# Kernel tuning notes

Hardware: AMD Instinct MI355X
Metric: run time of the kernel (lower is better)

The kernel has to match this reference:

```python
import jax, jax.numpy as jnp
import numpy as np

N_HEAD = 32
N_KV = 8
D = 2048
HD = D // N_HEAD
FF = 8192
EPS = 1e-5
THETA = 10000.0


def rms_norm(x, g):
    return g * x / jnp.sqrt(jnp.mean(x * x, axis=-1, keepdims=True) + EPS)


def rope(x):
    # x: [B, H, T, hd]; lucidrains interleaved RoPE
    T = x.shape[2]
    inv_freq = 1.0 / (THETA ** (jnp.arange(0, HD, 2, dtype=jnp.float32) / HD))  # [hd/2]
    freqs = jnp.arange(T, dtype=jnp.float32)[:, None] * inv_freq[None, :]       # [T, hd/2]
    freqs = jnp.repeat(freqs, 2, axis=-1)                                        # [T, hd]
    cos, sin = jnp.cos(freqs), jnp.sin(freqs)
    x1 = x[..., ::2]
    x2 = x[..., 1::2]
    rot = jnp.stack([-x2, x1], axis=-1).reshape(x.shape)
    return x * cos + rot * sin


def attention(x, wq, wk, wv, wo):
    B, T, C = x.shape
    q = (x @ wq).reshape(B, T, N_HEAD, HD).transpose(0, 2, 1, 3)  # [B,H,T,hd]
    k = (x @ wk).reshape(B, T, N_KV, HD).transpose(0, 2, 1, 3)    # [B,Hkv,T,hd]
    v = (x @ wv).reshape(B, T, N_KV, HD).transpose(0, 2, 1, 3)
    q = rope(q)
    k = rope(k)
    rep = N_HEAD // N_KV
    k = jnp.repeat(k, rep, axis=1)
    v = jnp.repeat(v, rep, axis=1)
    att = jnp.einsum('bhqd,bhkd->bhqk', q, k) * (1.0 / np.sqrt(HD))
    causal = jnp.tril(jnp.ones((T, T), dtype=bool))
    att = jnp.where(causal[None, None], att, -jnp.inf)
    att = jax.nn.softmax(att, axis=-1)
    y = jnp.einsum('bhqk,bhkd->bhqd', att, v)
    y = y.transpose(0, 2, 1, 3).reshape(B, T, C)
    return y @ wo


def mlp(x, wg, wu, wd):
    return (jax.nn.silu(x @ wg) * (x @ wu)) @ wd


def setup_inputs() -> dict:
    key = jax.random.key(0)
    ks = jax.random.split(key, 9)
    s = lambda fan_in: 1.0 / np.sqrt(fan_in)
    return {
        'x': jax.random.normal(ks[0], (1, 2048, D), dtype=jnp.float32),
        'g1': jnp.ones((D,), dtype=jnp.float32),
        'wq': jax.random.normal(ks[1], (D, D), dtype=jnp.float32) * s(D),
        'wk': jax.random.normal(ks[2], (D, N_KV * HD), dtype=jnp.float32) * s(D),
        'wv': jax.random.normal(ks[3], (D, N_KV * HD), dtype=jnp.float32) * s(D),
        'wo': jax.random.normal(ks[4], (D, D), dtype=jnp.float32) * s(D),
        'g2': jnp.ones((D,), dtype=jnp.float32),
        'wg': jax.random.normal(ks[5], (D, FF), dtype=jnp.float32) * s(D),
        'wu': jax.random.normal(ks[6], (D, FF), dtype=jnp.float32) * s(D),
        'wd': jax.random.normal(ks[7], (FF, D), dtype=jnp.float32) * s(FF),
    }


def reference(x, g1, wq, wk, wv, wo, g2, wg, wu, wd):
    residual = x
    x = rms_norm(x, g1)
    x = x + attention(x, wq, wk, wv, wo)
    x = rms_norm(x, g2)
    x = x + mlp(x, wg, wu, wd)
    x = x + residual
    return x
```

## Files before the change

### kernel.cpp

```cpp
#include <hip/hip_runtime.h>
#include <cstdint>
#include <cstddef>


typedef __attribute__((ext_vector_type(8))) short short8;
typedef __attribute__((ext_vector_type(4))) float f32x4;
typedef __attribute__((ext_vector_type(16))) float f32x16;

typedef __attribute__((address_space(1))) const void gvoid_t;
typedef __attribute__((address_space(3))) void lvoid_t;

__device__ inline unsigned short f2b(float f) {
  unsigned int u = __float_as_uint(f);
  u += 0x7fffu + ((u >> 16) & 1u);
  return (unsigned short)(u >> 16);
}
__device__ inline float b2f(unsigned short s) {
  return __uint_as_float((unsigned int)s << 16);
}
__device__ inline unsigned int pkbf(float lo, float hi) {
  unsigned int r;
  asm("v_cvt_pk_bf16_f32 %0, %1, %2" : "=v"(r) : "v"(lo), "v"(hi));
  return r;
}

__global__ __launch_bounds__(256) void transpose_cast(
    const float* __restrict__ W, unsigned short* __restrict__ Wt,
    int R, int ldW) {
  __shared__ unsigned short s[32 * 36];
  const int r0 = blockIdx.y * 32, c0 = blockIdx.x * 32;
  const int tr = threadIdx.x >> 3, tc = (threadIdx.x & 7) << 2;
  const float4 v = *(const float4*)(W + (size_t)(r0 + tr) * ldW + c0 + tc);
  s[tr * 36 + tc + 0] = f2b(v.x);
  s[tr * 36 + tc + 1] = f2b(v.y);
  s[tr * 36 + tc + 2] = f2b(v.z);
  s[tr * 36 + tc + 3] = f2b(v.w);
  __syncthreads();
  ushort4 o;
  o.x = s[(tc + 0) * 36 + tr];
  o.y = s[(tc + 1) * 36 + tr];
  o.z = s[(tc + 2) * 36 + tr];
  o.w = s[(tc + 3) * 36 + tr];
  *(ushort4*)(Wt + (size_t)(c0 + tr) * R + r0 + tc) = o;
}

__global__ __launch_bounds__(256) void rmsnorm(
    const float* __restrict__ X, const float* __restrict__ g,
    unsigned short* __restrict__ ob) {
  const int row = blockIdx.x;
  const float* x = X + (size_t)row * 2048;
  float ss = 0.f;
  for (int i = threadIdx.x; i < 2048; i += 256) { float v = x[i]; ss += v * v; }
  for (int off = 32; off; off >>= 1) ss += __shfl_down(ss, off, 64);
  __shared__ float red[4];
  if ((threadIdx.x & 63) == 0) red[threadIdx.x >> 6] = ss;
  __syncthreads();
  const float tot = red[0] + red[1] + red[2] + red[3];
  const float r = rsqrtf(tot * (1.f / 2048.f) + 1e-5f);
  for (int i = threadIdx.x; i < 2048; i += 256)
    ob[(size_t)row * 2048 + i] = f2b(x[i] * g[i] * r);
}

__global__ __launch_bounds__(256) void add_res(
    const unsigned short* __restrict__ h2, const float* __restrict__ x,
    float* __restrict__ out) {
  const int i = blockIdx.x * 256 + threadIdx.x;
  const ushort4 h = ((const ushort4*)h2)[i];
  const float4 xv = ((const float4*)x)[i];
  float4 o;
  o.x = xv.x + b2f(h.x); o.y = xv.y + b2f(h.y);
  o.z = xv.z + b2f(h.z); o.w = xv.w + b2f(h.w);
  ((float4*)out)[i] = o;
}

__global__ __launch_bounds__(256, 2) void gemm_bt(
    const unsigned short* __restrict__ A, const unsigned short* __restrict__ Bt,
    float* Cf, unsigned short* Cb,
    const unsigned short* add1b, const float* add2,
    int N, int Kfull, int Kchunk, int epi, int Tld,
    unsigned short* Cb2, unsigned short* Cb3) {
  __shared__ unsigned short As[128 * 64];
  __shared__ unsigned short Bs[128 * 64];
  const int tid = threadIdx.x;
  const int wave = tid >> 6, lane = tid & 63;
  const int quad = lane >> 4, l16 = lane & 15;
  const int m0 = blockIdx.y * 128, n0 = blockIdx.x * 128;
  const int wr = (wave >> 1) * 64, wc = (wave & 1) * 64;
  const int Ks = blockIdx.z * Kchunk, Ke = Ks + Kchunk;

  f32x4 acc[4][4] = {};

  for (int k0 = Ks; k0 < Ke; k0 += 64) {
#pragma unroll
    for (int p = 0; p < 4; ++p) {
      const int idx = p * 256 + tid;
      const int row = idx >> 3;
      const int kc = ((idx & 7) ^ (row & 7)) * 8;
      const unsigned short* gA = A + (size_t)(m0 + row) * Kfull + k0 + kc;
      const unsigned short* gB = Bt + (size_t)(n0 + row) * Kfull + k0 + kc;
      unsigned short* lA = As + (size_t)(p * 256 + wave * 64) * 8;
      unsigned short* lB = Bs + (size_t)(p * 256 + wave * 64) * 8;
      __builtin_amdgcn_global_load_lds((gvoid_t*)gA, (lvoid_t*)lA, 16, 0, 0);
      __builtin_amdgcn_global_load_lds((gvoid_t*)gB, (lvoid_t*)lB, 16, 0, 0);
    }
    __syncthreads();

#pragma unroll
    for (int ks = 0; ks < 2; ++ks) {
      short8 af[4], bf[4];
#pragma unroll
      for (int i = 0; i < 4; ++i) {
        const int row = wr + i * 16 + l16;
        af[i] = *(const short8*)(As + row * 64 +
                                 (((ks << 2) | quad) ^ (row & 7)) * 8);
      }
#pragma unroll
      for (int j = 0; j < 4; ++j) {
        const int row = wc + j * 16 + l16;
        bf[j] = *(const short8*)(Bs + row * 64 +
                                 (((ks << 2) | quad) ^ (row & 7)) * 8);
      }
#pragma unroll
      for (int i = 0; i < 4; ++i)
#pragma unroll
        for (int j = 0; j < 4; ++j)
          acc[i][j] = __builtin_amdgcn_mfma_f32_16x16x32_bf16(
              af[i], bf[j], acc[i][j], 0, 0, 0);
    }
    __syncthreads();
  }

  if (epi == 7 && n0 >= 2560) {
#pragma unroll
    for (int i = 0; i < 4; ++i)
#pragma unroll
      for (int j = 0; j < 4; ++j) {
        const int row = m0 + wr + i * 16 + quad * 4;
        const int col = n0 + wc + j * 16 + l16 - 2560;
        ushort4 o;
        o.x = f2b(acc[i][j][0]); o.y = f2b(acc[i][j][1]);
        o.z = f2b(acc[i][j][2]); o.w = f2b(acc[i][j][3]);
        *(ushort4*)(Cb3 + (size_t)col * Tld + row) = o;
      }
    return;
  }

#pragma unroll
  for (int i = 0; i < 4; ++i)
#pragma unroll
    for (int j = 0; j < 4; ++j) {
      const int rowb = m0 + wr + i * 16 + quad * 4;
      const int col = n0 + wc + j * 16 + l16;
      float invf = 0.f, sgn = 0.f;
      if (epi == 7) {
        const int ip = (col & 63) >> 1;
        invf = __expf(-(float)ip * 0.28782313662f);
        sgn = (col & 1) ? 1.f : -1.f;
      }
#pragma unroll
      for (int r = 0; r < 4; ++r) {
        const size_t idx = (size_t)(rowb + r) * N + col;
        const float v = acc[i][j][r];
        const float p = __shfl_xor(v, 1, 64);
        if (epi == 1) {
          Cf[idx] = v + b2f(add1b[idx]);
        } else if (epi == 3) {
          const float gt = b2f(add1b[idx]);
          Cb[idx] = f2b(gt / (1.f + __expf(-gt)) * v);
        } else if (epi == 4) {
          Cb[idx] = f2b(v);
        } else if (epi == 8) {
          atomicAdd(&Cf[idx], v);
        } else {
          float sn, cs;
          __sincosf((float)(rowb + r) * invf, &sn, &cs);
          const unsigned short o = f2b(v * cs + sgn * p * sn);
          if (col < 2048)
            Cb[(size_t)(rowb + r) * 2048 + col] = o;
          else
            Cb2[(size_t)(rowb + r) * 512 + col - 2048] = o;
        }
      }
    }
}

__global__ __launch_bounds__(256) void flash_attn(
    const unsigned short* __restrict__ Qb, const unsigned short* __restrict__ Kb,
    const unsigned short* __restrict__ Vt, unsigned short* __restrict__ Y,
    int T) {
  const int tid = threadIdx.x;
  const int wave = tid >> 6, lane = tid & 63;
  const int l32 = lane & 31, hi = lane >> 5;
  const int h = blockIdx.y, kvh = h >> 2;
  const int qt = (blockIdx.x + wave * 16) << 5;
  const int qrow = qt + l32;

  short8 qf[4];
#pragma unroll
  for (int ds = 0; ds < 4; ++ds) {
    short8 v = *(const short8*)(Qb + (size_t)qrow * 2048 + h * 64 +
                                ds * 16 + hi * 8);
#pragma unroll
    for (int e = 0; e < 8; ++e)
      v[e] = (short)f2b(b2f((unsigned short)v[e]) * 0.125f);
    qf[ds] = v;
  }

  const unsigned short* Kp = Kb + (size_t)l32 * 512 + kvh * 64 + hi * 8;
  const unsigned short* Vp = Vt + (size_t)(kvh * 64 + l32) * T + hi * 8;

  const int niter = (qt >> 5) + 1;
  float m_i = -3e38f, l_i = 0.f;
  f32x16 o0 = {}, o1 = {};

  short8 kf[4], kfn[4];
#pragma unroll
  for (int ds = 0; ds < 4; ++ds) kf[ds] = *(const short8*)(Kp + ds * 16);

  for (int it = 0; it < niter; ++it) {
    const int k0 = it << 5;
    short8 vf[2][2];
#pragma unroll
    for (int dt = 0; dt < 2; ++dt)
#pragma unroll
      for (int ks = 0; ks < 2; ++ks)
        vf[dt][ks] =
            *(const short8*)(Vp + (size_t)dt * 32 * T + k0 + ks * 16);
    const int kn = (k0 + 32 < 2016) ? k0 + 32 : 2016;
#pragma unroll
    for (int ds = 0; ds < 4; ++ds)
      kfn[ds] = *(const short8*)(Kp + (size_t)kn * 512 + ds * 16);

    f32x16 S = {};
#pragma unroll
    for (int ds = 0; ds < 4; ++ds)
      S = __builtin_amdgcn_mfma_f32_32x32x16_bf16(kf[ds], qf[ds], S, 0, 0, 0);

    float s[16];
#pragma unroll
    for (int r = 0; r < 16; ++r) s[r] = S[r];
    if (k0 == qt) {
#pragma unroll
      for (int r = 0; r < 16; ++r)
        if (((r & 3) + 8 * (r >> 2) + 4 * hi) > l32) s[r] = -3e38f;
    }

    float tmax = s[0];
#pragma unroll
    for (int r = 1; r < 16; ++r) tmax = fmaxf(tmax, s[r]);
    tmax = fmaxf(tmax, __shfl_xor(tmax, 32, 64));

    if (!__all(tmax <= m_i + 8.f)) {
      const float mn = fmaxf(m_i, tmax);
      const float al = __expf(m_i - mn);
#pragma unroll
      for (int r = 0; r < 16; ++r) { o0[r] *= al; o1[r] *= al; }
      l_i *= al;
      m_i = mn;
    }

    float p[16], rs = 0.f;
#pragma unroll
    for (int r = 0; r < 16; ++r) { p[r] = __expf(s[r] - m_i); rs += p[r]; }
    rs += __shfl_xor(rs, 32, 64);
    l_i += rs;

    short8 pf[2];
#pragma unroll
    for (int ks = 0; ks < 2; ++ks) {
      const int rb = ks * 8;
      const unsigned int a0 = pkbf(p[rb + 0], p[rb + 1]);
      const unsigned int a1 = pkbf(p[rb + 2], p[rb + 3]);
      const unsigned int b0 = pkbf(p[rb + 4], p[rb + 5]);
      const unsigned int b1 = pkbf(p[rb + 6], p[rb + 7]);
      const unsigned int t0 = __shfl_xor((int)(hi ? a0 : b0), 32, 64);
      const unsigned int t1 = __shfl_xor((int)(hi ? a1 : b1), 32, 64);
      union { unsigned int u[4]; short8 v; } pu;
      pu.u[0] = hi ? t0 : a0;
      pu.u[1] = hi ? t1 : a1;
      pu.u[2] = hi ? b0 : t0;
      pu.u[3] = hi ? b1 : t1;
      pf[ks] = pu.v;
    }

#pragma unroll
    for (int ks = 0; ks < 2; ++ks) {
      o0 = __builtin_amdgcn_mfma_f32_32x32x16_bf16(vf[0][ks], pf[ks], o0,
                                                   0, 0, 0);
      o1 = __builtin_amdgcn_mfma_f32_32x32x16_bf16(vf[1][ks], pf[ks], o1,
                                                   0, 0, 0);
    }
#pragma unroll
    for (int ds = 0; ds < 4; ++ds) kf[ds] = kfn[ds];
  }

  const float inv = 1.f / l_i;
  unsigned short* Yp = Y + (size_t)qrow * 2048 + h * 64 + hi * 4;
#pragma unroll
  for (int g = 0; g < 4; ++g) {
    ushort4 u0, u1;
    u0.x = f2b(o0[g * 4 + 0] * inv); u0.y = f2b(o0[g * 4 + 1] * inv);
    u0.z = f2b(o0[g * 4 + 2] * inv); u0.w = f2b(o0[g * 4 + 3] * inv);
    *(ushort4*)(Yp + g * 8) = u0;
    u1.x = f2b(o1[g * 4 + 0] * inv); u1.y = f2b(o1[g * 4 + 1] * inv);
    u1.z = f2b(o1[g * 4 + 2] * inv); u1.w = f2b(o1[g * 4 + 3] * inv);
    *(ushort4*)(Yp + 32 + g * 8) = u1;
  }
}

extern "C" void kernel_launch(void* const* d_in, const int* in_sizes, int n_in,
                              void* d_out, int out_size, void* d_ws,
                              size_t ws_size, hipStream_t stream) {
  const float* x  = (const float*)d_in[0];
  const float* g1 = (const float*)d_in[1];
  const float* wq = (const float*)d_in[2];
  const float* wk = (const float*)d_in[3];
  const float* wv = (const float*)d_in[4];
  const float* wo = (const float*)d_in[5];
  const float* g2 = (const float*)d_in[6];
  const float* wg = (const float*)d_in[7];
  const float* wu = (const float*)d_in[8];
  const float* wd = (const float*)d_in[9];
  float* out = (float*)d_out;

  const int T = 2048, Dm = 2048, FF = 8192;
  char* ws = (char*)d_ws;
  const size_t MB = (size_t)1 << 20;

  unsigned short* wq_t = (unsigned short*)(ws + 0 * MB);
  unsigned short* wk_t = (unsigned short*)(ws + 8 * MB);
  unsigned short* wv_t = (unsigned short*)(ws + 10 * MB);
  unsigned short* wo_t = (unsigned short*)(ws + 12 * MB);
  unsigned short* wg_t = (unsigned short*)(ws + 20 * MB);
  unsigned short* wu_t = (unsigned short*)(ws + 52 * MB);
  unsigned short* h1_b = (unsigned short*)(ws + 84 * MB);
  unsigned short* h2_b = (unsigned short*)(ws + 92 * MB);
  float*          x2_f = (float*)(ws + 100 * MB);
  unsigned short* gate = (unsigned short*)(ws + 100 * MB);
  unsigned short* q_b  = (unsigned short*)(ws + 132 * MB);
  unsigned short* k_b  = (unsigned short*)(ws + 140 * MB);
  unsigned short* vt_b = (unsigned short*)(ws + 142 * MB);
  unsigned short* y_b  = (unsigned short*)(ws + 144 * MB);
  unsigned short* wd_t = (unsigned short*)(ws + 132 * MB);

  transpose_cast<<<dim3(64, 64), 256, 0, stream>>>(wq, wq_t, Dm, Dm);
  transpose_cast<<<dim3(16, 64), 256, 0, stream>>>(wk, wk_t, Dm, 512);
  transpose_cast<<<dim3(16, 64), 256, 0, stream>>>(wv, wv_t, Dm, 512);
  transpose_cast<<<dim3(64, 64), 256, 0, stream>>>(wo, wo_t, Dm, Dm);
  transpose_cast<<<dim3(256, 64), 256, 0, stream>>>(wg, wg_t, Dm, FF);
  transpose_cast<<<dim3(256, 64), 256, 0, stream>>>(wu, wu_t, Dm, FF);

  rmsnorm<<<T, 256, 0, stream>>>(x, g1, h1_b);

  gemm_bt<<<dim3(24, 16), 256, 0, stream>>>(h1_b, wq_t, nullptr, q_b, nullptr,
                                            nullptr, 3072, Dm, Dm, 7, T, k_b,
                                            vt_b);

  flash_attn<<<dim3(16, 32), 256, 0, stream>>>(q_b, k_b, vt_b, y_b, T);

  gemm_bt<<<dim3(16, 16), 256, 0, stream>>>(y_b, wo_t, x2_f, nullptr, h1_b,
                                            nullptr, Dm, Dm, Dm, 1, 0, nullptr,
                                            nullptr);

  transpose_cast<<<dim3(64, 256), 256, 0, stream>>>(wd, wd_t, FF, Dm);

  rmsnorm<<<T, 256, 0, stream>>>(x2_f, g2, h2_b);

  gemm_bt<<<dim3(64, 16), 256, 0, stream>>>(h2_b, wg_t, nullptr, gate, nullptr,
                                            nullptr, FF, Dm, Dm, 4, 0, nullptr,
                                            nullptr);
  gemm_bt<<<dim3(64, 16), 256, 0, stream>>>(h2_b, wu_t, nullptr, gate, gate,
                                            nullptr, FF, Dm, Dm, 3, 0, nullptr,
                                            nullptr);

  add_res<<<(T * Dm / 4) / 256, 256, 0, stream>>>(h2_b, x, out);
  gemm_bt<<<dim3(16, 16, 4), 256, 0, stream>>>(gate, wd_t, out, nullptr,
                                               nullptr, nullptr, Dm, FF,
                                               FF / 4, 8, 0, nullptr, nullptr);
}
```

Baseline: 721.4 us.

## Add 256x256-tile pipelined GEMM kernel for MLP projections

Adds a new 512-thread GEMM kernel with 256x256 output tiles, a 64-wide K step and double-buffered LDS. Tiles are staged with direct global-to-LDS loads using an XOR swizzle, and MFMA work is interleaved in quarters with the prefetch of the next K tile, using barriers and priority hints. The gate, up and down MLP projections now use this kernel in place of the older gemm_bt. The larger tile raises data reuse per block but gives fewer blocks (256 for gate/up, 256 for down with split-K), which may underfill the GPU and relies on tight vmcnt and barrier accounting.

```diff
diff --git a/kernel.cpp b/kernel.cpp
--- a/kernel.cpp
+++ b/kernel.cpp
@@ -23,6 +23,13 @@
   asm("v_cvt_pk_bf16_f32 %0, %1, %2" : "=v"(r) : "v"(lo), "v"(hi));
   return r;
 }
+
+#define SBAR()                                  \
+  do {                                          \
+    asm volatile("" ::: "memory");              \
+    __builtin_amdgcn_s_barrier();               \
+    asm volatile("" ::: "memory");              \
+  } while (0)
 
 __global__ __launch_bounds__(256) void transpose_cast(
     const float* __restrict__ W, unsigned short* __restrict__ Wt,
@@ -184,6 +191,187 @@
     }
 }
 
+__device__ __forceinline__ void stage_half(
+    const unsigned short* __restrict__ G, int ldg, unsigned short* L,
+    int k0, int wave) {
+  const int lane = threadIdx.x & 63;
+#pragma unroll
+  for (int l = 0; l < 2; ++l) {
+    const int idx = l * 512 + wave * 64 + lane;
+    const int row = idx >> 3;
+    const int kc = ((idx & 7) ^ (row & 7)) << 3;
+    const unsigned short* g = G + (size_t)row * ldg + k0 + kc;
+    unsigned short* lp = L + (size_t)(l * 512 + wave * 64) * 8;
+    __builtin_amdgcn_global_load_lds((gvoid_t*)g, (lvoid_t*)lp, 16, 0, 0);
+  }
+}
+
+__global__ __launch_bounds__(512, 2) void gemm256(
+    const unsigned short* __restrict__ A, const unsigned short* __restrict__ Bt,
+    float* Cf, unsigned short* Cb, const unsigned short* add1b,
+    int N, int Kfull, int Kchunk, int epi) {
+  __shared__ unsigned short As[2][256 * 64];
+  __shared__ unsigned short Bs[2][256 * 64];
+  const int tid = threadIdx.x;
+  const int wave = tid >> 6, lane = tid & 63;
+  const int quad = lane >> 4, l16 = lane & 15;
+  const int wm = wave >> 2, wn = wave & 3;
+  const int m0 = blockIdx.y * 256, n0 = blockIdx.x * 256;
+  const int Ks = blockIdx.z * Kchunk;
+  const int NT = Kchunk >> 6;
+
+  const unsigned short* Ag = A + (size_t)m0 * Kfull + Ks;
+  const unsigned short* Bg = Bt + (size_t)n0 * Kfull + Ks;
+  const size_t hstep = (size_t)128 * Kfull;
+
+  f32x4 acc[8][4] = {};
+
+  stage_half(Ag, Kfull, &As[0][0], 0, wave);
+  stage_half(Ag + hstep, Kfull, &As[0][128 * 64], 0, wave);
+  stage_half(Bg, Kfull, &Bs[0][0], 0, wave);
+  stage_half(Bg + hstep, Kfull, &Bs[0][128 * 64], 0, wave);
+  if (NT > 1) {
+    stage_half(Bg, Kfull, &Bs[1][0], 64, wave);
+    stage_half(Bg + hstep, Kfull, &Bs[1][128 * 64], 64, wave);
+    asm volatile("s_waitcnt vmcnt(4)" ::: "memory");
+  } else {
+    asm volatile("s_waitcnt vmcnt(0)" ::: "memory");
+  }
+  SBAR();
+
+  const int cbank = ((quad) ^ (l16 & 7)) * 8;
+
+  for (int u = 0; u < NT; ++u) {
+    const unsigned short* Asb = &As[u & 1][0];
+    const unsigned short* Bsb = &Bs[u & 1][0];
+    unsigned short* Asn = &As[(u + 1) & 1][0];
+    unsigned short* Bsn = &Bs[u & 1][0];
+    const int k1 = (u + 1) << 6, k2 = (u + 2) << 6;
+
+    short8 af[4][2], bf0[2][2], bf1[2][2];
+
+#pragma unroll
+    for (int ii = 0; ii < 4; ++ii)
+#pragma unroll
+      for (int ks = 0; ks < 2; ++ks) {
+        const int row = wm * 128 + ii * 16 + l16;
+        af[ii][ks] = *(const short8*)(
+            Asb + row * 64 + ((((ks << 2) | quad) ^ (l16 & 7)) << 3));
+      }
+#pragma unroll
+    for (int j = 0; j < 2; ++j)
+#pragma unroll
+      for (int ks = 0; ks < 2; ++ks) {
+        const int row = wn * 64 + j * 16 + l16;
+        bf0[j][ks] = *(const short8*)(
+            Bsb + row * 64 + ((((ks << 2) | quad) ^ (l16 & 7)) << 3));
+      }
+    if (u + 1 < NT) stage_half(Ag, Kfull, Asn, k1, wave);
+    SBAR();
+    asm volatile("s_waitcnt lgkmcnt(0)" ::: "memory");
+    __builtin_amdgcn_sched_barrier(0);
+    __builtin_amdgcn_s_setprio(1);
+#pragma unroll
+    for (int ii = 0; ii < 4; ++ii)
+#pragma unroll
+      for (int j = 0; j < 2; ++j)
+#pragma unroll
+        for (int ks = 0; ks < 2; ++ks)
+          acc[ii][j] = __builtin_amdgcn_mfma_f32_16x16x32_bf16(
+              af[ii][ks], bf0[j][ks], acc[ii][j], 0, 0, 0);
+    __builtin_amdgcn_s_setprio(0);
+    SBAR();
+
+#pragma unroll
+    for (int j = 0; j < 2; ++j)
+#pragma unroll
+      for (int ks = 0; ks < 2; ++ks) {
+        const int row = wn * 64 + (2 + j) * 16 + l16;
+        bf1[j][ks] = *(const short8*)(
+            Bsb + row * 64 + ((((ks << 2) | quad) ^ (l16 & 7)) << 3));
+      }
+    if (u + 1 < NT) stage_half(Ag + hstep, Kfull, Asn + 128 * 64, k1, wave);
+    SBAR();
+    asm volatile("s_waitcnt lgkmcnt(0)" ::: "memory");
+    __builtin_amdgcn_sched_barrier(0);
+    __builtin_amdgcn_s_setprio(1);
+#pragma unroll
+    for (int ii = 0; ii < 4; ++ii)
+#pragma unroll
+      for (int j = 0; j < 2; ++j)
+#pragma unroll
+        for (int ks = 0; ks < 2; ++ks)
+          acc[ii][2 + j] = __builtin_amdgcn_mfma_f32_16x16x32_bf16(
+              af[ii][ks], bf1[j][ks], acc[ii][2 + j], 0, 0, 0);
+    __builtin_amdgcn_s_setprio(0);
+    SBAR();
+
+#pragma unroll
+    for (int ii = 0; ii < 4; ++ii)
+#pragma unroll
+      for (int ks = 0; ks < 2; ++ks) {
+        const int row = wm * 128 + (4 + ii) * 16 + l16;
+        af[ii][ks] = *(const short8*)(
+            Asb + row * 64 + ((((ks << 2) | quad) ^ (l16 & 7)) << 3));
+      }
+    if (u + 2 < NT) stage_half(Bg, Kfull, Bsn, k2, wave);
+    SBAR();
+    asm volatile("s_waitcnt lgkmcnt(0)" ::: "memory");
+    __builtin_amdgcn_sched_barrier(0);
+    __builtin_amdgcn_s_setprio(1);
+#pragma unroll
+    for (int ii = 0; ii < 4; ++ii)
+#pragma unroll
+      for (int j = 0; j < 2; ++j)
+#pragma unroll
+        for (int ks = 0; ks < 2; ++ks)
+          acc[4 + ii][j] = __builtin_amdgcn_mfma_f32_16x16x32_bf16(
+              af[ii][ks], bf0[j][ks], acc[4 + ii][j], 0, 0, 0);
+    __builtin_amdgcn_s_setprio(0);
+    SBAR();
+
+    if (u + 2 < NT) stage_half(Bg + hstep, Kfull, Bsn + 128 * 64, k2, wave);
+    SBAR();
+    __builtin_amdgcn_s_setprio(1);
+#pragma unroll
+    for (int ii = 0; ii < 4; ++ii)
+#pragma unroll
+      for (int j = 0; j < 2; ++j)
+#pragma unroll
+        for (int ks = 0; ks < 2; ++ks)
+          acc[4 + ii][2 + j] = __builtin_amdgcn_mfma_f32_16x16x32_bf16(
+              af[ii][ks], bf1[j][ks], acc[4 + ii][2 + j], 0, 0, 0);
+    __builtin_amdgcn_s_setprio(0);
+    if (u + 2 < NT) {
+      asm volatile("s_waitcnt vmcnt(4)" ::: "memory");
+    } else if (u + 1 < NT) {
+      asm volatile("s_waitcnt vmcnt(0)" ::: "memory");
+    }
+    SBAR();
+  }
+
+#pragma unroll
+  for (int i = 0; i < 8; ++i)
+#pragma unroll
+    for (int j = 0; j < 4; ++j) {
+      const int rowb = m0 + wm * 128 + i * 16 + quad * 4;
+      const int col = n0 + wn * 64 + j * 16 + l16;
+#pragma unroll
+      for (int r = 0; r < 4; ++r) {
+        const size_t idx = (size_t)(rowb + r) * N + col;
+        const float v = acc[i][j][r];
+        if (epi == 3) {
+          const float gt = b2f(add1b[idx]);
+          Cb[idx] = f2b(gt / (1.f + __expf(-gt)) * v);
+        } else if (epi == 4) {
+          Cb[idx] = f2b(v);
+        } else {
+          atomicAdd(&Cf[idx], v);
+        }
+      }
+    }
+}
+
 __global__ __launch_bounds__(256) void flash_attn(
     const unsigned short* __restrict__ Qb, const unsigned short* __restrict__ Kb,
     const unsigned short* __restrict__ Vt, unsigned short* __restrict__ Y,
@@ -366,15 +554,12 @@
 
   rmsnorm<<<T, 256, 0, stream>>>(x2_f, g2, h2_b);
 
-  gemm_bt<<<dim3(64, 16), 256, 0, stream>>>(h2_b, wg_t, nullptr, gate, nullptr,
-                                            nullptr, FF, Dm, Dm, 4, 0, nullptr,
-                                            nullptr);
-  gemm_bt<<<dim3(64, 16), 256, 0, stream>>>(h2_b, wu_t, nullptr, gate, gate,
-                                            nullptr, FF, Dm, Dm, 3, 0, nullptr,
-                                            nullptr);
+  gemm256<<<dim3(32, 8), 512, 0, stream>>>(h2_b, wg_t, nullptr, gate, nullptr,
+                                           FF, Dm, Dm, 4);
+  gemm256<<<dim3(32, 8), 512, 0, stream>>>(h2_b, wu_t, nullptr, gate, gate,
+                                           FF, Dm, Dm, 3);
 
   add_res<<<(T * Dm / 4) / 256, 256, 0, stream>>>(h2_b, x, out);
-  gemm_bt<<<dim3(16, 16, 4), 256, 0, stream>>>(gate, wd_t, out, nullptr,
-                                               nullptr, nullptr, Dm, FF,
-                                               FF / 4, 8, 0, nullptr, nullptr);
-}
+  gemm256<<<dim3(8, 8, 4), 512, 0, stream>>>(gate, wd_t, out, nullptr, nullptr,
+                                             Dm, FF, FF / 4, 8);
+}
```

Result: slower. 770.2 us (+6.8%).

## Fuse gate and up projections into one GEMM kernel and swizzle blocks across XCDs

Applied to the files above, without the earlier changes.

Replaces the two MLP gate/up GEMM launches with a single kernel that loads each A tile once and computes both gate and up accumulators, applying SiLU*up in the epilogue. This removes a full re-read of the activations, the bf16 round-trip of the gate intermediate, and one launch. It also adds an XCD-aware block index remap to the GEMMs to improve L2 locality. The fused kernel doubles accumulator registers and uses 48KB of LDS, which may reduce occupancy and leaves the global-to-LDS loads unpipelined.

```diff
diff --git a/kernel.cpp b/kernel.cpp
--- a/kernel.cpp
+++ b/kernel.cpp
@@ -22,6 +22,15 @@
   unsigned int r;
   asm("v_cvt_pk_bf16_f32 %0, %1, %2" : "=v"(r) : "v"(lo), "v"(hi));
   return r;
+}
+
+__device__ inline void xcd_swz(int& bx, int& by) {
+  const int nbx = gridDim.x;
+  const int nwg = nbx * gridDim.y;
+  int f = by * nbx + bx;
+  f = (f & 7) * (nwg >> 3) + (f >> 3);
+  bx = f % nbx;
+  by = f / nbx;
 }
 
 __global__ __launch_bounds__(256) void transpose_cast(
@@ -84,7 +93,9 @@
   const int tid = threadIdx.x;
   const int wave = tid >> 6, lane = tid & 63;
   const int quad = lane >> 4, l16 = lane & 15;
-  const int m0 = blockIdx.y * 128, n0 = blockIdx.x * 128;
+  int bx = blockIdx.x, by = blockIdx.y;
+  xcd_swz(bx, by);
+  const int m0 = by * 128, n0 = bx * 128;
   const int wr = (wave >> 1) * 64, wc = (wave & 1) * 64;
   const int Ks = blockIdx.z * Kchunk, Ke = Ks + Kchunk;
 
@@ -164,13 +175,13 @@
         const float p = __shfl_xor(v, 1, 64);
         if (epi == 1) {
           Cf[idx] = v + b2f(add1b[idx]);
+        } else if (epi == 8) {
+          atomicAdd(&Cf[idx], v);
+        } else if (epi == 4) {
+          Cb[idx] = f2b(v);
         } else if (epi == 3) {
           const float gt = b2f(add1b[idx]);
           Cb[idx] = f2b(gt / (1.f + __expf(-gt)) * v);
-        } else if (epi == 4) {
-          Cb[idx] = f2b(v);
-        } else if (epi == 8) {
-          atomicAdd(&Cf[idx], v);
         } else {
           float sn, cs;
           __sincosf((float)(rowb + r) * invf, &sn, &cs);
@@ -180,6 +191,85 @@
           else
             Cb2[(size_t)(rowb + r) * 512 + col - 2048] = o;
         }
+      }
+    }
+}
+
+__global__ __launch_bounds__(256, 2) void gemm_gu(
+    const unsigned short* __restrict__ A, const unsigned short* __restrict__ Bg,
+    const unsigned short* __restrict__ Bu, unsigned short* __restrict__ act,
+    int N, int K) {
+  __shared__ unsigned short As[128 * 64];
+  __shared__ unsigned short Gs[128 * 64];
+  __shared__ unsigned short Us[128 * 64];
+  const int tid = threadIdx.x;
+  const int wave = tid >> 6, lane = tid & 63;
+  const int quad = lane >> 4, l16 = lane & 15;
+  int bx = blockIdx.x, by = blockIdx.y;
+  xcd_swz(bx, by);
+  const int m0 = by * 128, n0 = bx * 128;
+  const int wr = (wave >> 1) * 64, wc = (wave & 1) * 64;
+
+  f32x4 aG[4][4] = {}, aU[4][4] = {};
+
+  for (int k0 = 0; k0 < K; k0 += 64) {
+#pragma unroll
+    for (int p = 0; p < 4; ++p) {
+      const int idx = p * 256 + tid;
+      const int row = idx >> 3;
+      const int kc = ((idx & 7) ^ (row & 7)) * 8;
+      const size_t off = (size_t)(p * 256 + wave * 64) * 8;
+      __builtin_amdgcn_global_load_lds(
+          (gvoid_t*)(A + (size_t)(m0 + row) * K + k0 + kc),
+          (lvoid_t*)(As + off), 16, 0, 0);
+      __builtin_amdgcn_global_load_lds(
+          (gvoid_t*)(Bg + (size_t)(n0 + row) * K + k0 + kc),
+          (lvoid_t*)(Gs + off), 16, 0, 0);
+      __builtin_amdgcn_global_load_lds(
+          (gvoid_t*)(Bu + (size_t)(n0 + row) * K + k0 + kc),
+          (lvoid_t*)(Us + off), 16, 0, 0);
+    }
+    __syncthreads();
+
+#pragma unroll
+    for (int ks = 0; ks < 2; ++ks) {
+      short8 af[4], bg[4], bu[4];
+#pragma unroll
+      for (int i = 0; i < 4; ++i) {
+        const int row = wr + i * 16 + l16;
+        af[i] = *(const short8*)(As + row * 64 +
+                                 (((ks << 2) | quad) ^ (row & 7)) * 8);
+      }
+#pragma unroll
+      for (int j = 0; j < 4; ++j) {
+        const int row = wc + j * 16 + l16;
+        const int kk = (((ks << 2) | quad) ^ (row & 7)) * 8;
+        bg[j] = *(const short8*)(Gs + row * 64 + kk);
+        bu[j] = *(const short8*)(Us + row * 64 + kk);
+      }
+#pragma unroll
+      for (int i = 0; i < 4; ++i)
+#pragma unroll
+        for (int j = 0; j < 4; ++j) {
+          aG[i][j] = __builtin_amdgcn_mfma_f32_16x16x32_bf16(
+              af[i], bg[j], aG[i][j], 0, 0, 0);
+          aU[i][j] = __builtin_amdgcn_mfma_f32_16x16x32_bf16(
+              af[i], bu[j], aU[i][j], 0, 0, 0);
+        }
+    }
+    __syncthreads();
+  }
+
+#pragma unroll
+  for (int i = 0; i < 4; ++i)
+#pragma unroll
+    for (int j = 0; j < 4; ++j) {
+      const int rowb = m0 + wr + i * 16 + quad * 4;
+      const int col = n0 + wc + j * 16 + l16;
+#pragma unroll
+      for (int r = 0; r < 4; ++r) {
+        const float g = aG[i][j][r], u = aU[i][j][r];
+        act[(size_t)(rowb + r) * N + col] = f2b(g / (1.f + __expf(-g)) * u);
       }
     }
 }
@@ -366,12 +456,7 @@
 
   rmsnorm<<<T, 256, 0, stream>>>(x2_f, g2, h2_b);
 
-  gemm_bt<<<dim3(64, 16), 256, 0, stream>>>(h2_b, wg_t, nullptr, gate, nullptr,
-                                            nullptr, FF, Dm, Dm, 4, 0, nullptr,
-                                            nullptr);
-  gemm_bt<<<dim3(64, 16), 256, 0, stream>>>(h2_b, wu_t, nullptr, gate, gate,
-                                            nullptr, FF, Dm, Dm, 3, 0, nullptr,
-                                            nullptr);
+  gemm_gu<<<dim3(64, 16), 256, 0, stream>>>(h2_b, wg_t, wu_t, gate, FF, Dm);
 
   add_res<<<(T * Dm / 4) / 256, 256, 0, stream>>>(h2_b, x, out);
   gemm_bt<<<dim3(16, 16, 4), 256, 0, stream>>>(gate, wd_t, out, nullptr,
```

New measurement: 724.7 us. No clear change (+0.4%).
